# Performance work log

Hardware: AMD Instinct MI355X
Metric: run time of the kernel (lower is better)

The kernel has to match this reference:

```python
import jax, jax.numpy as jnp
import numpy as np

N = 16384   # nodes
E = 262144  # edges (avg degree 16)
H = 256     # hidden_dim
R = 32      # num_radial


def _lin(k, fi, fo):
    return jax.random.normal(k, (fi, fo), jnp.float32) / np.float32(np.sqrt(fi))


def setup_inputs() -> dict:
    key = jax.random.key(0)
    ks = jax.random.split(key, 16)
    h = jax.random.normal(ks[0], (N, H), jnp.float32)
    pos = jax.random.normal(ks[1], (N, 3), jnp.float32)
    edge_index = jax.random.randint(ks[2], (2, E), 0, N, dtype=jnp.int32)
    return {
        'h': h, 'pos': pos,
        # radial_basis: Linear(1,R), SiLU, Linear(R,R)
        'rb_w1': _lin(ks[3], 1, R), 'rb_b1': jnp.zeros((R,), jnp.float32),
        'rb_w2': _lin(ks[4], R, R), 'rb_b2': jnp.zeros((R,), jnp.float32),
        # edge_network: Linear(2H+R,H), SiLU, Linear(H,H), LayerNorm(H)
        'en_w1': _lin(ks[5], 2 * H + R, H), 'en_b1': jnp.zeros((H,), jnp.float32),
        'en_w2': _lin(ks[6], H, H), 'en_b2': jnp.zeros((H,), jnp.float32),
        'en_g': jnp.ones((H,), jnp.float32), 'en_bt': jnp.zeros((H,), jnp.float32),
        # node_network: Linear(2H,H), SiLU, Linear(H,H), LayerNorm(H)
        'nn_w1': _lin(ks[7], 2 * H, H), 'nn_b1': jnp.zeros((H,), jnp.float32),
        'nn_w2': _lin(ks[8], H, H), 'nn_b2': jnp.zeros((H,), jnp.float32),
        'nn_g': jnp.ones((H,), jnp.float32), 'nn_bt': jnp.zeros((H,), jnp.float32),
        # coord_network: Linear(H,H//2), SiLU, Linear(H//2,1), Tanh
        'cn_w1': _lin(ks[9], H, H // 2), 'cn_b1': jnp.zeros((H // 2,), jnp.float32),
        'cn_w2': _lin(ks[10], H // 2, 1), 'cn_b2': jnp.zeros((1,), jnp.float32),
        'edge_index': edge_index,
    }


def _ln(x, g, b, eps=1e-5):
    mu = jnp.mean(x, axis=-1, keepdims=True)
    var = jnp.var(x, axis=-1, keepdims=True)
    return (x - mu) / jnp.sqrt(var + eps) * g + b


def reference(h, pos, rb_w1, rb_b1, rb_w2, rb_b2,
              en_w1, en_b1, en_w2, en_b2, en_g, en_bt,
              nn_w1, nn_b1, nn_w2, nn_b2, nn_g, nn_bt,
              cn_w1, cn_b1, cn_w2, cn_b2, edge_index):
    row, col = edge_index[0], edge_index[1]
    rel_pos = pos[col] - pos[row]                                   # [E,3]
    # torch: norm(rel_pos + 1e-8) -> scalar eps added to the vector first
    dist = jnp.linalg.norm(rel_pos + 1e-8, axis=-1, keepdims=True)  # [E,1]
    radial = jax.nn.silu(dist @ rb_w1 + rb_b1) @ rb_w2 + rb_b2      # [E,R]
    edge_feat = jnp.concatenate([h[row], h[col], radial], axis=-1)  # [E,2H+R]
    edge_msg = _ln(jax.nn.silu(edge_feat @ en_w1 + en_b1) @ en_w2 + en_b2,
                   en_g, en_bt)                                     # [E,H]
    # PyG propagate with aggr='add': sum messages at target nodes (col)
    node_msg = jax.ops.segment_sum(edge_msg, col, num_segments=h.shape[0])
    hn_in = jnp.concatenate([h, node_msg], axis=-1)                 # [N,2H]
    h_updated = _ln(jax.nn.silu(hn_in @ nn_w1 + nn_b1) @ nn_w2 + nn_b2,
                    nn_g, nn_bt)                                    # [N,H]
    coord_w = jnp.tanh(jax.nn.silu(edge_msg @ cn_w1 + cn_b1) @ cn_w2 + cn_b2)  # [E,1]
    weighted = rel_pos * coord_w                                    # [E,3]
    pos_updates = jnp.zeros_like(pos).at[row].add(-weighted).at[col].add(weighted)
    return h_updated, pos_updates
```

## Files before the change

### kernel.cpp

```cpp
#include <hip/hip_runtime.h>
#include <hip/hip_bf16.h>


#define NN 16384
#define EE 262144
#define HH 256
#define RR 32

typedef __bf16 bf16x8 __attribute__((ext_vector_type(8)));
typedef float f32x4 __attribute__((ext_vector_type(4)));

__device__ __forceinline__ float silu_f(float x) { return x / (1.0f + __expf(-x)); }

__device__ __forceinline__ unsigned short bf_bits(float x) {
  union { __hip_bfloat16 b; unsigned short u; } v;
  v.b = __float2bfloat16(x);
  return v.u;
}
__device__ __forceinline__ float ubf(unsigned short u) {
  return __uint_as_float(((unsigned)u) << 16);
}

__global__ __launch_bounds__(256) void conv_h_kernel(const float* __restrict__ src,
                                                     __hip_bfloat16* __restrict__ dst,
                                                     int n4) {
  int i = blockIdx.x * 256 + threadIdx.x;
  if (i >= n4) return;
  float4 v = ((const float4*)src)[i];
  __hip_bfloat16* d = dst + (size_t)i * 4;
  d[0] = __float2bfloat16(v.x);
  d[1] = __float2bfloat16(v.y);
  d[2] = __float2bfloat16(v.z);
  d[3] = __float2bfloat16(v.w);
}

__global__ __launch_bounds__(256) void tr_kernel(const float* __restrict__ in,
                                                 __hip_bfloat16* __restrict__ out,
                                                 int K, int Nc) {
  int i = blockIdx.x * 256 + threadIdx.x;
  if (i >= K * Nc) return;
  int k = i / Nc, c = i - k * Nc;
  out[(size_t)c * K + k] = __float2bfloat16(in[i]);
}

__global__ __launch_bounds__(256) void rwt_kernel(const float* __restrict__ rb_w2,
                                                  const float* __restrict__ en_w1,
                                                  __hip_bfloat16* __restrict__ RWT) {
  int t = blockIdx.x * 256 + threadIdx.x;
  if (t >= 256 * 32) return;
  int c = t >> 5, i = t & 31;
  float s = 0.f;
#pragma unroll
  for (int j = 0; j < 32; ++j) s += rb_w2[i * 32 + j] * en_w1[(512 + j) * 256 + c];
  RWT[c * 32 + i] = __float2bfloat16(s);
}

__global__ __launch_bounds__(256) void b1p_kernel(const float* __restrict__ en_b1,
                                                  const float* __restrict__ rb_b2,
                                                  const float* __restrict__ en_w1,
                                                  float* __restrict__ b1p) {
  int c = blockIdx.x * 256 + threadIdx.x;
  if (c >= 256) return;
  float s = en_b1[c];
#pragma unroll
  for (int j = 0; j < 32; ++j) s += rb_b2[j] * en_w1[(512 + j) * 256 + c];
  b1p[c] = s;
}

__global__ __launch_bounds__(256) void count_kernel(const int* __restrict__ ei,
                                                    int* __restrict__ counts) {
  int e = blockIdx.x * 256 + threadIdx.x;
  if (e >= EE) return;
  atomicAdd(&counts[ei[EE + e]], 1);
}

__global__ __launch_bounds__(256) void scanA_kernel(const int* __restrict__ counts,
                                                    int* __restrict__ bsum) {
  __shared__ int ws[4];
  int t = threadIdx.x;
  int v = counts[blockIdx.x * 256 + t];
#pragma unroll
  for (int m = 1; m < 64; m <<= 1) v += __shfl_xor(v, m, 64);
  if ((t & 63) == 0) ws[t >> 6] = v;
  __syncthreads();
  if (t == 0) bsum[blockIdx.x] = ws[0] + ws[1] + ws[2] + ws[3];
}

__global__ __launch_bounds__(64) void scanB_kernel(const int* __restrict__ bsum,
                                                   int* __restrict__ bbase,
                                                   int* __restrict__ offs) {
  int t = threadIdx.x;
  int v = bsum[t], x = v;
#pragma unroll
  for (int d = 1; d < 64; d <<= 1) {
    int y = __shfl_up(x, d, 64);
    if (t >= d) x += y;
  }
  bbase[t] = x - v;
  if (t == 63) offs[NN] = x;
}

__global__ __launch_bounds__(256) void scanC_kernel(const int* __restrict__ counts,
                                                    const int* __restrict__ bbase,
                                                    int* __restrict__ offs,
                                                    int* __restrict__ cursor) {
  __shared__ int wtot[4];
  int t = threadIdx.x, wv = t >> 6, ln = t & 63;
  int base = blockIdx.x * 256;
  int v = counts[base + t], x = v;
#pragma unroll
  for (int d = 1; d < 64; d <<= 1) {
    int y = __shfl_up(x, d, 64);
    if (ln >= d) x += y;
  }
  if (ln == 63) wtot[wv] = x;
  __syncthreads();
  int add = bbase[blockIdx.x];
  for (int k = 0; k < wv; ++k) add += wtot[k];
  int excl = add + x - v;
  offs[base + t] = excl;
  cursor[base + t] = excl;
}

__global__ __launch_bounds__(256) void scatter_kernel(const int* __restrict__ ei,
                                                      int* __restrict__ cursor,
                                                      int* __restrict__ elist) {
  int e = blockIdx.x * 256 + threadIdx.x;
  if (e >= EE) return;
  int c = ei[EE + e];
  int p = atomicAdd(&cursor[c], 1);
  elist[p] = e;
}

__global__ __launch_bounds__(512) void pgemm_kernel(const __hip_bfloat16* __restrict__ A,
                                                    const __hip_bfloat16* __restrict__ BT,
                                                    __hip_bfloat16* __restrict__ out) {
  const int tid = threadIdx.x, w = tid >> 6, l = tid & 63, r = l & 15, g = l >> 4;
  const int n0 = blockIdx.x * 64;
  f32x4 acc[4][4];
#pragma unroll
  for (int a = 0; a < 4; ++a)
#pragma unroll
    for (int b = 0; b < 4; ++b) acc[a][b] = (f32x4){0.f, 0.f, 0.f, 0.f};
  for (int ks = 0; ks < 8; ++ks) {
    bf16x8 af[4], bfr[4];
#pragma unroll
    for (int fm = 0; fm < 4; ++fm)
      af[fm] = *(const bf16x8*)(A + (size_t)(n0 + fm * 16 + r) * 256 + ks * 32 + g * 8);
#pragma unroll
    for (int fn = 0; fn < 4; ++fn)
      bfr[fn] = *(const bf16x8*)(BT + (size_t)(w * 64 + fn * 16 + r) * 256 + ks * 32 + g * 8);
#pragma unroll
    for (int fm = 0; fm < 4; ++fm)
#pragma unroll
      for (int fn = 0; fn < 4; ++fn)
        acc[fm][fn] =
            __builtin_amdgcn_mfma_f32_16x16x32_bf16(af[fm], bfr[fn], acc[fm][fn], 0, 0, 0);
  }
#pragma unroll
  for (int fm = 0; fm < 4; ++fm)
#pragma unroll
    for (int fn = 0; fn < 4; ++fn) {
      int col = w * 64 + fn * 16 + r;
#pragma unroll
      for (int q = 0; q < 4; ++q) {
        int row = n0 + fm * 16 + g * 4 + q;
        out[(size_t)row * 512 + col] = __float2bfloat16(acc[fm][fn][q]);
      }
    }
}

__global__ __launch_bounds__(512, 4) void edge_kernel(
    const __hip_bfloat16* __restrict__ Pb, const int* __restrict__ ei,
    const float* __restrict__ pos, const float* __restrict__ rb_w1,
    const float* __restrict__ rb_b1, const __hip_bfloat16* __restrict__ RWT,
    const float* __restrict__ b1p, const __hip_bfloat16* __restrict__ W2T,
    const float* __restrict__ en_b2, const float* __restrict__ en_g,
    const float* __restrict__ en_bt, const __hip_bfloat16* __restrict__ CW1T,
    const float* __restrict__ cn_b1, const float* __restrict__ cn_w2,
    const float* __restrict__ cn_b2, const int* __restrict__ elist,
    __hip_bfloat16* __restrict__ emsg, float* __restrict__ pos_out) {
  __shared__ __align__(16) __hip_bfloat16 A2[64 * 264];
  __shared__ float relb[64][3];
  __shared__ float distb[64];
  __shared__ int srow[64], scol[64];
  __shared__ float red[8][64], redsq[8][64];
  __shared__ float mv[64][2];
  __shared__ float cb1b[128], cw2b[128];

  const int tid = threadIdx.x, w = tid >> 6, l = tid & 63, r = l & 15, g = l >> 4;
  const int e0 = blockIdx.x * 64;

  if (tid < 128) {
    cb1b[tid] = cn_b1[tid];
    cw2b[tid] = cn_w2[tid];
  }
  if (tid < 64) {
    int e = elist[e0 + tid];
    int r2 = ei[e], c2 = ei[EE + e];
    srow[tid] = r2;
    scol[tid] = c2;
    float dx = pos[c2 * 3 + 0] - pos[r2 * 3 + 0];
    float dy = pos[c2 * 3 + 1] - pos[r2 * 3 + 1];
    float dz = pos[c2 * 3 + 2] - pos[r2 * 3 + 2];
    relb[tid][0] = dx;
    relb[tid][1] = dy;
    relb[tid][2] = dz;
    float ex = dx + 1e-8f, ey = dy + 1e-8f, ez = dz + 1e-8f;
    distb[tid] = sqrtf(ex * ex + ey * ey + ez * ez);
  }
  __syncthreads();

  unsigned short* A2u = (unsigned short*)A2;
  {
    const int eloc = (w & 3) * 16 + r;
    const int chalf = w >> 2;
    float d = distb[eloc];
    bf16x8 sfrag;
#pragma unroll
    for (int j = 0; j < 8; ++j) {
      float x = d * rb_w1[g * 8 + j] + rb_b1[g * 8 + j];
      sfrag[j] = (__bf16)silu_f(x);
    }
#pragma unroll
    for (int t = 0; t < 8; ++t) {
      int cblk = chalf * 8 + t;
      int cbase = cblk * 16 + g * 4;
      bf16x8 afr = *(const bf16x8*)(RWT + (size_t)(cblk * 16 + r) * 32 + g * 8);
      f32x4 rad = __builtin_amdgcn_mfma_f32_16x16x32_bf16(
          afr, sfrag, (f32x4){0.f, 0.f, 0.f, 0.f}, 0, 0, 0);
      ushort4 o;
      o.x = bf_bits(rad[0]);
      o.y = bf_bits(rad[1]);
      o.z = bf_bits(rad[2]);
      o.w = bf_bits(rad[3]);
      *(ushort4*)(A2u + (size_t)eloc * 264 + cbase) = o;
    }
  }
  __syncthreads();

#pragma unroll
  for (int it = 0; it < 4; ++it) {
    int ch = it * 512 + tid;
    int i = ch >> 5, c = ch & 31;
    bf16x8 radv = *(const bf16x8*)(A2 + i * 264 + c * 8);
    bf16x8 p1 = *(const bf16x8*)(Pb + (size_t)srow[i] * 512 + c * 8);
    bf16x8 p2 = *(const bf16x8*)(Pb + (size_t)scol[i] * 512 + 256 + c * 8);
    float4 b1a = *(const float4*)(b1p + c * 8);
    float4 b1b = *(const float4*)(b1p + c * 8 + 4);
    float bv[8] = {b1a.x, b1a.y, b1a.z, b1a.w, b1b.x, b1b.y, b1b.z, b1b.w};
    bf16x8 o;
#pragma unroll
    for (int j = 0; j < 8; ++j)
      o[j] = (__bf16)silu_f((float)radv[j] + (float)p1[j] + (float)p2[j] + bv[j]);
    *(bf16x8*)(A2 + i * 264 + c * 8) = o;
  }
  __syncthreads();

  f32x4 acc[2][4];
#pragma unroll
  for (int a = 0; a < 2; ++a)
#pragma unroll
    for (int b = 0; b < 4; ++b) acc[a][b] = (f32x4){0.f, 0.f, 0.f, 0.f};
  for (int ks = 0; ks < 8; ++ks) {
    bf16x8 af[2], bfr[4];
#pragma unroll
    for (int mf = 0; mf < 2; ++mf)
      af[mf] = *(const bf16x8*)(W2T + (size_t)(w * 32 + mf * 16 + r) * 256 + ks * 32 + g * 8);
#pragma unroll
    for (int nf = 0; nf < 4; ++nf)
      bfr[nf] = *(const bf16x8*)(A2 + (nf * 16 + r) * 264 + ks * 32 + g * 8);
#pragma unroll
    for (int mf = 0; mf < 2; ++mf)
#pragma unroll
      for (int nf = 0; nf < 4; ++nf)
        acc[mf][nf] =
            __builtin_amdgcn_mfma_f32_16x16x32_bf16(af[mf], bfr[nf], acc[mf][nf], 0, 0, 0);
  }
  {
    float4 b2v0 = *(const float4*)(en_b2 + w * 32 + g * 4);
    float4 b2v1 = *(const float4*)(en_b2 + w * 32 + 16 + g * 4);
#pragma unroll
    for (int nf = 0; nf < 4; ++nf) {
      acc[0][nf][0] += b2v0.x;
      acc[0][nf][1] += b2v0.y;
      acc[0][nf][2] += b2v0.z;
      acc[0][nf][3] += b2v0.w;
      acc[1][nf][0] += b2v1.x;
      acc[1][nf][1] += b2v1.y;
      acc[1][nf][2] += b2v1.z;
      acc[1][nf][3] += b2v1.w;
    }
  }

#pragma unroll
  for (int nf = 0; nf < 4; ++nf) {
    float s = 0.f, sq = 0.f;
#pragma unroll
    for (int mf = 0; mf < 2; ++mf)
#pragma unroll
      for (int q = 0; q < 4; ++q) {
        float v = acc[mf][nf][q];
        s += v;
        sq += v * v;
      }
    s += __shfl_xor(s, 16, 64);
    s += __shfl_xor(s, 32, 64);
    sq += __shfl_xor(sq, 16, 64);
    sq += __shfl_xor(sq, 32, 64);
    if (l < 16) {
      red[w][nf * 16 + l] = s;
      redsq[w][nf * 16 + l] = sq;
    }
  }
  __syncthreads();
  if (tid < 64) {
    float s = 0.f, sq = 0.f;
#pragma unroll
    for (int k = 0; k < 8; ++k) {
      s += red[k][tid];
      sq += redsq[k][tid];
    }
    float mean = s * (1.0f / HH);
    float var = sq * (1.0f / HH) - mean * mean;
    mv[tid][0] = mean;
    mv[tid][1] = rsqrtf(var + 1e-5f);
  }
  __syncthreads();

  {
    float4 gv0 = *(const float4*)(en_g + w * 32 + g * 4);
    float4 gv1 = *(const float4*)(en_g + w * 32 + 16 + g * 4);
    float4 bv0 = *(const float4*)(en_bt + w * 32 + g * 4);
    float4 bv1 = *(const float4*)(en_bt + w * 32 + 16 + g * 4);
#pragma unroll
    for (int nf = 0; nf < 4; ++nf) {
      int e = nf * 16 + r;
      float mm = mv[e][0], rs = mv[e][1];
      ushort4 o0, o1;
      o0.x = bf_bits((acc[0][nf][0] - mm) * rs * gv0.x + bv0.x);
      o0.y = bf_bits((acc[0][nf][1] - mm) * rs * gv0.y + bv0.y);
      o0.z = bf_bits((acc[0][nf][2] - mm) * rs * gv0.z + bv0.z);
      o0.w = bf_bits((acc[0][nf][3] - mm) * rs * gv0.w + bv0.w);
      o1.x = bf_bits((acc[1][nf][0] - mm) * rs * gv1.x + bv1.x);
      o1.y = bf_bits((acc[1][nf][1] - mm) * rs * gv1.y + bv1.y);
      o1.z = bf_bits((acc[1][nf][2] - mm) * rs * gv1.z + bv1.z);
      o1.w = bf_bits((acc[1][nf][3] - mm) * rs * gv1.w + bv1.w);
      *(ushort4*)(A2u + (size_t)e * 264 + w * 32 + g * 4) = o0;
      *(ushort4*)(A2u + (size_t)e * 264 + w * 32 + 16 + g * 4) = o1;
    }
  }
  __syncthreads();

#pragma unroll
  for (int it = 0; it < 4; ++it) {
    int ch = it * 512 + tid;
    int i = ch >> 5, c = ch & 31;
    *(float4*)(emsg + (size_t)(e0 + i) * HH + c * 8) = *(const float4*)(A2 + i * 264 + c * 8);
  }

  f32x4 c2a[4];
#pragma unroll
  for (int a = 0; a < 4; ++a) c2a[a] = (f32x4){0.f, 0.f, 0.f, 0.f};
  for (int ks = 0; ks < 8; ++ks) {
    bf16x8 af[4];
#pragma unroll
    for (int fm = 0; fm < 4; ++fm)
      af[fm] = *(const bf16x8*)(A2 + (fm * 16 + r) * 264 + ks * 32 + g * 8);
    bf16x8 bfr = *(const bf16x8*)(CW1T + (size_t)(w * 16 + r) * 256 + ks * 32 + g * 8);
#pragma unroll
    for (int fm = 0; fm < 4; ++fm)
      c2a[fm] = __builtin_amdgcn_mfma_f32_16x16x32_bf16(af[fm], bfr, c2a[fm], 0, 0, 0);
  }
  {
    int ccol = w * 16 + r;
    float cb = cb1b[ccol], cw = cw2b[ccol];
#pragma unroll
    for (int fm = 0; fm < 4; ++fm)
#pragma unroll
      for (int q = 0; q < 4; ++q) {
        float v = silu_f(c2a[fm][q] + cb) * cw;
#pragma unroll
        for (int m = 1; m < 16; m <<= 1) v += __shfl_xor(v, m, 64);
        if (r == 0) red[w][fm * 16 + g * 4 + q] = v;
      }
  }
  __syncthreads();
  if (tid < 64) {
    float s = cn_b2[0];
#pragma unroll
    for (int k = 0; k < 8; ++k) s += red[k][tid];
    float wgt = tanhf(s);
    float ax = relb[tid][0], ay = relb[tid][1], az = relb[tid][2];
    int rr = srow[tid], cc = scol[tid];
    atomicAdd(&pos_out[rr * 3 + 0], -wgt * ax);
    atomicAdd(&pos_out[rr * 3 + 1], -wgt * ay);
    atomicAdd(&pos_out[rr * 3 + 2], -wgt * az);
    atomicAdd(&pos_out[cc * 3 + 0], wgt * ax);
    atomicAdd(&pos_out[cc * 3 + 1], wgt * ay);
    atomicAdd(&pos_out[cc * 3 + 2], wgt * az);
  }
}

__global__ __launch_bounds__(256) void nodemsg_kernel(const int* __restrict__ offs,
                                                      const __hip_bfloat16* __restrict__ emsg,
                                                      __hip_bfloat16* __restrict__ nmsgb) {
  int wid = threadIdx.x >> 6, l = threadIdx.x & 63;
  int n = blockIdx.x * 4 + wid;
  float a0 = 0.f, a1 = 0.f, a2 = 0.f, a3 = 0.f;
  int b = offs[n], e2 = offs[n + 1];
  const unsigned short* E = (const unsigned short*)emsg;
  int p = b;
  for (; p + 1 < e2; p += 2) {
    ushort4 va = *(const ushort4*)(E + (size_t)p * HH + l * 4);
    ushort4 vb = *(const ushort4*)(E + (size_t)(p + 1) * HH + l * 4);
    a0 += ubf(va.x) + ubf(vb.x);
    a1 += ubf(va.y) + ubf(vb.y);
    a2 += ubf(va.z) + ubf(vb.z);
    a3 += ubf(va.w) + ubf(vb.w);
  }
  if (p < e2) {
    ushort4 va = *(const ushort4*)(E + (size_t)p * HH + l * 4);
    a0 += ubf(va.x);
    a1 += ubf(va.y);
    a2 += ubf(va.z);
    a3 += ubf(va.w);
  }
  ushort4 o;
  o.x = bf_bits(a0);
  o.y = bf_bits(a1);
  o.z = bf_bits(a2);
  o.w = bf_bits(a3);
  *(ushort4*)((unsigned short*)nmsgb + (size_t)n * HH + l * 4) = o;
}

__global__ __launch_bounds__(512, 4) void node_kernel(
    const __hip_bfloat16* __restrict__ hb, const __hip_bfloat16* __restrict__ nmsgb,
    const __hip_bfloat16* __restrict__ NW1T, const float* __restrict__ nn_b1,
    const __hip_bfloat16* __restrict__ NW2T, const float* __restrict__ nn_b2,
    const float* __restrict__ nn_g, const float* __restrict__ nn_bt,
    float* __restrict__ out_h) {
  __shared__ __align__(16) __hip_bfloat16 A2[32 * 264];
  __shared__ float red[8][32], redsq[8][32];
  __shared__ float mv[32][2];
  __shared__ float gb[HH], btb[HH];
  const int tid = threadIdx.x, w = tid >> 6, l = tid & 63, r = l & 15, g = l >> 4;
  const int n0 = blockIdx.x * 32;
  if (tid < 256) {
    gb[tid] = nn_g[tid];
    btb[tid] = nn_bt[tid];
  }

  f32x4 acc[2][2];
#pragma unroll
  for (int a = 0; a < 2; ++a)
#pragma unroll
    for (int b = 0; b < 2; ++b) acc[a][b] = (f32x4){0.f, 0.f, 0.f, 0.f};
  for (int ks = 0; ks < 8; ++ks) {
    bf16x8 af[2], bfr[2];
#pragma unroll
    for (int fm = 0; fm < 2; ++fm)
      af[fm] = *(const bf16x8*)(hb + (size_t)(n0 + fm * 16 + r) * 256 + ks * 32 + g * 8);
#pragma unroll
    for (int fn = 0; fn < 2; ++fn)
      bfr[fn] = *(const bf16x8*)(NW1T + (size_t)(w * 32 + fn * 16 + r) * 512 + ks * 32 + g * 8);
#pragma unroll
    for (int fm = 0; fm < 2; ++fm)
#pragma unroll
      for (int fn = 0; fn < 2; ++fn)
        acc[fm][fn] =
            __builtin_amdgcn_mfma_f32_16x16x32_bf16(af[fm], bfr[fn], acc[fm][fn], 0, 0, 0);
  }
  for (int ks = 0; ks < 8; ++ks) {
    bf16x8 af[2], bfr[2];
#pragma unroll
    for (int fm = 0; fm < 2; ++fm)
      af[fm] = *(const bf16x8*)(nmsgb + (size_t)(n0 + fm * 16 + r) * 256 + ks * 32 + g * 8);
#pragma unroll
    for (int fn = 0; fn < 2; ++fn)
      bfr[fn] =
          *(const bf16x8*)(NW1T + (size_t)(w * 32 + fn * 16 + r) * 512 + 256 + ks * 32 + g * 8);
#pragma unroll
    for (int fm = 0; fm < 2; ++fm)
#pragma unroll
      for (int fn = 0; fn < 2; ++fn)
        acc[fm][fn] =
            __builtin_amdgcn_mfma_f32_16x16x32_bf16(af[fm], bfr[fn], acc[fm][fn], 0, 0, 0);
  }
  __syncthreads();
#pragma unroll
  for (int fn = 0; fn < 2; ++fn) {
    int col = w * 32 + fn * 16 + r;
    float b1 = nn_b1[col];
#pragma unroll
    for (int fm = 0; fm < 2; ++fm)
#pragma unroll
      for (int q = 0; q < 4; ++q) {
        int row = fm * 16 + g * 4 + q;
        A2[row * 264 + col] = __float2bfloat16(silu_f(acc[fm][fn][q] + b1));
      }
  }
  __syncthreads();

#pragma unroll
  for (int a = 0; a < 2; ++a)
#pragma unroll
    for (int b = 0; b < 2; ++b) acc[a][b] = (f32x4){0.f, 0.f, 0.f, 0.f};
  for (int ks = 0; ks < 8; ++ks) {
    bf16x8 af[2], bfr[2];
#pragma unroll
    for (int fm = 0; fm < 2; ++fm)
      af[fm] = *(const bf16x8*)(A2 + (fm * 16 + r) * 264 + ks * 32 + g * 8);
#pragma unroll
    for (int fn = 0; fn < 2; ++fn)
      bfr[fn] = *(const bf16x8*)(NW2T + (size_t)(w * 32 + fn * 16 + r) * 256 + ks * 32 + g * 8);
#pragma unroll
    for (int fm = 0; fm < 2; ++fm)
#pragma unroll
      for (int fn = 0; fn < 2; ++fn)
        acc[fm][fn] =
            __builtin_amdgcn_mfma_f32_16x16x32_bf16(af[fm], bfr[fn], acc[fm][fn], 0, 0, 0);
  }
#pragma unroll
  for (int fn = 0; fn < 2; ++fn) {
    float b2 = nn_b2[w * 32 + fn * 16 + r];
#pragma unroll
    for (int fm = 0; fm < 2; ++fm)
#pragma unroll
      for (int q = 0; q < 4; ++q) acc[fm][fn][q] += b2;
  }
#pragma unroll
  for (int fm = 0; fm < 2; ++fm)
#pragma unroll
    for (int q = 0; q < 4; ++q) {
      float s = acc[fm][0][q] + acc[fm][1][q];
      float sq = acc[fm][0][q] * acc[fm][0][q] + acc[fm][1][q] * acc[fm][1][q];
#pragma unroll
      for (int m = 1; m < 16; m <<= 1) {
        s += __shfl_xor(s, m, 64);
        sq += __shfl_xor(sq, m, 64);
      }
      if (r == 0) {
        red[w][fm * 16 + g * 4 + q] = s;
        redsq[w][fm * 16 + g * 4 + q] = sq;
      }
    }
  __syncthreads();
  if (tid < 32) {
    float s = 0.f, sq = 0.f;
#pragma unroll
    for (int k = 0; k < 8; ++k) {
      s += red[k][tid];
      sq += redsq[k][tid];
    }
    float mean = s * (1.0f / HH);
    float var = sq * (1.0f / HH) - mean * mean;
    mv[tid][0] = mean;
    mv[tid][1] = rsqrtf(var + 1e-5f);
  }
  __syncthreads();
#pragma unroll
  for (int fn = 0; fn < 2; ++fn) {
    int col = w * 32 + fn * 16 + r;
    float gg = gb[col], bb = btb[col];
#pragma unroll
    for (int fm = 0; fm < 2; ++fm)
#pragma unroll
      for (int q = 0; q < 4; ++q) {
        int row = fm * 16 + g * 4 + q;
        out_h[(size_t)(n0 + row) * HH + col] =
            (acc[fm][fn][q] - mv[row][0]) * mv[row][1] * gg + bb;
      }
  }
}

extern "C" void kernel_launch(void* const* d_in, const int* in_sizes, int n_in,
                              void* d_out, int out_size, void* d_ws, size_t ws_size,
                              hipStream_t stream) {
  const float* h = (const float*)d_in[0];
  const float* pos = (const float*)d_in[1];
  const float* rb_w1 = (const float*)d_in[2];
  const float* rb_b1 = (const float*)d_in[3];
  const float* rb_w2 = (const float*)d_in[4];
  const float* rb_b2 = (const float*)d_in[5];
  const float* en_w1 = (const float*)d_in[6];
  const float* en_b1 = (const float*)d_in[7];
  const float* en_w2 = (const float*)d_in[8];
  const float* en_b2 = (const float*)d_in[9];
  const float* en_g = (const float*)d_in[10];
  const float* en_bt = (const float*)d_in[11];
  const float* nn_w1 = (const float*)d_in[12];
  const float* nn_b1 = (const float*)d_in[13];
  const float* nn_w2 = (const float*)d_in[14];
  const float* nn_b2 = (const float*)d_in[15];
  const float* nn_g = (const float*)d_in[16];
  const float* nn_bt = (const float*)d_in[17];
  const float* cn_w1 = (const float*)d_in[18];
  const float* cn_b1 = (const float*)d_in[19];
  const float* cn_w2 = (const float*)d_in[20];
  const float* cn_b2 = (const float*)d_in[21];
  const int* ei = (const int*)d_in[22];

  float* out_h = (float*)d_out;
  float* out_pos = out_h + (size_t)NN * HH;

  char* p = (char*)d_ws;
  auto alloc = [&p](size_t bytes) {
    char* q = p;
    p += (bytes + 255) & ~(size_t)255;
    return q;
  };
  __hip_bfloat16* hb = (__hip_bfloat16*)alloc((size_t)NN * HH * 2);
  __hip_bfloat16* Pb = (__hip_bfloat16*)alloc((size_t)NN * 512 * 2);
  __hip_bfloat16* W1abT = (__hip_bfloat16*)alloc((size_t)512 * 256 * 2);
  __hip_bfloat16* W2T = (__hip_bfloat16*)alloc((size_t)256 * 256 * 2);
  __hip_bfloat16* NW1T = (__hip_bfloat16*)alloc((size_t)256 * 512 * 2);
  __hip_bfloat16* NW2T = (__hip_bfloat16*)alloc((size_t)256 * 256 * 2);
  __hip_bfloat16* CW1T = (__hip_bfloat16*)alloc((size_t)128 * 256 * 2);
  __hip_bfloat16* RWT = (__hip_bfloat16*)alloc((size_t)256 * 32 * 2);
  float* b1p = (float*)alloc((size_t)256 * 4);
  __hip_bfloat16* emsg = (__hip_bfloat16*)alloc((size_t)EE * HH * 2);
  __hip_bfloat16* nmsgb = (__hip_bfloat16*)alloc((size_t)NN * HH * 2);
  int* counts = (int*)alloc((size_t)NN * 4);
  int* offs = (int*)alloc((size_t)(NN + 1) * 4);
  int* cursor = (int*)alloc((size_t)NN * 4);
  int* elist = (int*)alloc((size_t)EE * 4);
  int* bsum = (int*)alloc((size_t)64 * 4);
  int* bbase = (int*)alloc((size_t)64 * 4);

  hipMemsetAsync(out_pos, 0, (size_t)NN * 3 * sizeof(float), stream);
  hipMemsetAsync(counts, 0, (size_t)NN * sizeof(int), stream);

  conv_h_kernel<<<(NN * HH / 4 + 255) / 256, 256, 0, stream>>>(h, hb, NN * HH / 4);
  tr_kernel<<<(256 * 256) / 256, 256, 0, stream>>>(en_w2, W2T, 256, 256);
  tr_kernel<<<(512 * 256) / 256, 256, 0, stream>>>(nn_w1, NW1T, 512, 256);
  tr_kernel<<<(256 * 256) / 256, 256, 0, stream>>>(nn_w2, NW2T, 256, 256);
  tr_kernel<<<(256 * 128) / 256, 256, 0, stream>>>(cn_w1, CW1T, 256, 128);
  tr_kernel<<<(256 * 256) / 256, 256, 0, stream>>>(en_w1, W1abT, 256, 256);
  tr_kernel<<<(256 * 256) / 256, 256, 0, stream>>>(en_w1 + 256 * 256, W1abT + 256 * 256, 256,
                                                   256);
  rwt_kernel<<<(256 * 32) / 256, 256, 0, stream>>>(rb_w2, en_w1, RWT);
  b1p_kernel<<<1, 256, 0, stream>>>(en_b1, rb_b2, en_w1, b1p);
  count_kernel<<<EE / 256, 256, 0, stream>>>(ei, counts);
  scanA_kernel<<<NN / 256, 256, 0, stream>>>(counts, bsum);
  scanB_kernel<<<1, 64, 0, stream>>>(bsum, bbase, offs);
  scanC_kernel<<<NN / 256, 256, 0, stream>>>(counts, bbase, offs, cursor);
  scatter_kernel<<<EE / 256, 256, 0, stream>>>(ei, cursor, elist);
  pgemm_kernel<<<NN / 64, 512, 0, stream>>>(hb, W1abT, Pb);
  edge_kernel<<<EE / 64, 512, 0, stream>>>(Pb, ei, pos, rb_w1, rb_b1, RWT, b1p, W2T, en_b2,
                                           en_g, en_bt, CW1T, cn_b1, cn_w2, cn_b2, elist,
                                           emsg, out_pos);
  nodemsg_kernel<<<NN / 4, 256, 0, stream>>>(offs, emsg, nmsgb);
  node_kernel<<<NN / 32, 512, 0, stream>>>(hb, nmsgb, NW1T, nn_b1, NW2T, nn_b2, nn_g, nn_bt,
                                           out_h);
}
```

Measured before the change: 513.0 us.

## Split edge kernel, fuse segment-sum via atomics, merge weight prep kernels

Merges the weight transpose/prep launches into one kernel. Splits the edge kernel into a hidden-activation kernel that writes a swizzled bf16 buffer and a message kernel that loads it into LDS with global_load_lds. The message kernel reduces sorted-by-target rows in LDS and atomically adds fp32 partial sums into a zeroed node-message buffer, replacing the separate nodemsg pass and the per-edge message write. It also swaps the coord GEMM operand roles and uses XOR swizzle instead of padding. The trade-off is a new E×H intermediate round trip and extra atomics and memset.

```diff
diff --git a/kernel.cpp b/kernel.cpp
--- a/kernel.cpp
+++ b/kernel.cpp
@@ -9,6 +9,13 @@
 
 typedef __bf16 bf16x8 __attribute__((ext_vector_type(8)));
 typedef float f32x4 __attribute__((ext_vector_type(4)));
+
+typedef const void __attribute__((address_space(1)))* gas_ptr;
+typedef void __attribute__((address_space(3)))* las_ptr;
+
+__device__ __forceinline__ void gload16(const void* g, void* l) {
+  __builtin_amdgcn_global_load_lds((gas_ptr)g, (las_ptr)l, 16, 0, 0);
+}
 
 __device__ __forceinline__ float silu_f(float x) { return x / (1.0f + __expf(-x)); }
 
@@ -34,37 +41,48 @@
   d[3] = __float2bfloat16(v.w);
 }
 
-__global__ __launch_bounds__(256) void tr_kernel(const float* __restrict__ in,
-                                                 __hip_bfloat16* __restrict__ out,
-                                                 int K, int Nc) {
-  int i = blockIdx.x * 256 + threadIdx.x;
-  if (i >= K * Nc) return;
-  int k = i / Nc, c = i - k * Nc;
-  out[(size_t)c * K + k] = __float2bfloat16(in[i]);
-}
-
-__global__ __launch_bounds__(256) void rwt_kernel(const float* __restrict__ rb_w2,
-                                                  const float* __restrict__ en_w1,
-                                                  __hip_bfloat16* __restrict__ RWT) {
-  int t = blockIdx.x * 256 + threadIdx.x;
-  if (t >= 256 * 32) return;
-  int c = t >> 5, i = t & 31;
-  float s = 0.f;
-#pragma unroll
-  for (int j = 0; j < 32; ++j) s += rb_w2[i * 32 + j] * en_w1[(512 + j) * 256 + c];
-  RWT[c * 32 + i] = __float2bfloat16(s);
-}
-
-__global__ __launch_bounds__(256) void b1p_kernel(const float* __restrict__ en_b1,
-                                                  const float* __restrict__ rb_b2,
-                                                  const float* __restrict__ en_w1,
-                                                  float* __restrict__ b1p) {
-  int c = blockIdx.x * 256 + threadIdx.x;
-  if (c >= 256) return;
-  float s = en_b1[c];
-#pragma unroll
-  for (int j = 0; j < 32; ++j) s += rb_b2[j] * en_w1[(512 + j) * 256 + c];
-  b1p[c] = s;
+__global__ __launch_bounds__(256) void prep_w_kernel(
+    const float* __restrict__ en_w1, const float* __restrict__ en_w2,
+    const float* __restrict__ nn_w1, const float* __restrict__ nn_w2,
+    const float* __restrict__ cn_w1, const float* __restrict__ rb_w2,
+    const float* __restrict__ rb_b2, const float* __restrict__ en_b1,
+    __hip_bfloat16* __restrict__ W2T, __hip_bfloat16* __restrict__ NW1T,
+    __hip_bfloat16* __restrict__ NW2T, __hip_bfloat16* __restrict__ CW1T,
+    __hip_bfloat16* __restrict__ W1abT, __hip_bfloat16* __restrict__ RWT,
+    float* __restrict__ b1p) {
+  int bid = blockIdx.x, tid = threadIdx.x;
+  if (bid < 256) {
+    int i = bid * 256 + tid, k = i >> 8, c = i & 255;
+    W2T[(size_t)c * 256 + k] = __float2bfloat16(en_w2[i]);
+  } else if (bid < 768) {
+    int i = (bid - 256) * 256 + tid, k = i >> 8, c = i & 255;
+    NW1T[(size_t)c * 512 + k] = __float2bfloat16(nn_w1[i]);
+  } else if (bid < 1024) {
+    int i = (bid - 768) * 256 + tid, k = i >> 8, c = i & 255;
+    NW2T[(size_t)c * 256 + k] = __float2bfloat16(nn_w2[i]);
+  } else if (bid < 1152) {
+    int i = (bid - 1024) * 256 + tid, k = i >> 7, c = i & 127;
+    CW1T[(size_t)c * 256 + k] = __float2bfloat16(cn_w1[i]);
+  } else if (bid < 1408) {
+    int i = (bid - 1152) * 256 + tid, k = i >> 8, c = i & 255;
+    W1abT[(size_t)c * 256 + k] = __float2bfloat16(en_w1[i]);
+  } else if (bid < 1664) {
+    int i = (bid - 1408) * 256 + tid, k = i >> 8, c = i & 255;
+    W1abT[(size_t)(256 + c) * 256 + k] = __float2bfloat16(en_w1[256 * 256 + i]);
+  } else if (bid < 1696) {
+    int t = (bid - 1664) * 256 + tid;
+    int c = t >> 5, i = t & 31;
+    float s = 0.f;
+#pragma unroll
+    for (int j = 0; j < 32; ++j) s += rb_w2[i * 32 + j] * en_w1[(512 + j) * 256 + c];
+    RWT[c * 32 + i] = __float2bfloat16(s);
+  } else {
+    int c = tid;
+    float s = en_b1[c];
+#pragma unroll
+    for (int j = 0; j < 32; ++j) s += rb_b2[j] * en_w1[(512 + j) * 256 + c];
+    b1p[c] = s;
+  }
 }
 
 __global__ __launch_bounds__(256) void count_kernel(const int* __restrict__ ei,
@@ -170,90 +188,79 @@
     }
 }
 
-__global__ __launch_bounds__(512, 4) void edge_kernel(
+__global__ __launch_bounds__(256, 4) void hidden_kernel(
     const __hip_bfloat16* __restrict__ Pb, const int* __restrict__ ei,
     const float* __restrict__ pos, const float* __restrict__ rb_w1,
     const float* __restrict__ rb_b1, const __hip_bfloat16* __restrict__ RWT,
-    const float* __restrict__ b1p, const __hip_bfloat16* __restrict__ W2T,
+    const float* __restrict__ b1p, const int* __restrict__ elist,
+    __hip_bfloat16* __restrict__ hiddenb) {
+  const int tid = threadIdx.x, w = tid >> 6, l = tid & 63, r = l & 15, g = l >> 4;
+  const int slot = blockIdx.x * 64 + w * 16 + r;
+  int e = elist[slot];
+  int nr = ei[e], nc = ei[EE + e];
+  float dx = pos[nc * 3 + 0] - pos[nr * 3 + 0] + 1e-8f;
+  float dy = pos[nc * 3 + 1] - pos[nr * 3 + 1] + 1e-8f;
+  float dz = pos[nc * 3 + 2] - pos[nr * 3 + 2] + 1e-8f;
+  float d = sqrtf(dx * dx + dy * dy + dz * dz);
+  bf16x8 sfrag;
+#pragma unroll
+  for (int j = 0; j < 8; ++j) {
+    float x = d * rb_w1[g * 8 + j] + rb_b1[g * 8 + j];
+    sfrag[j] = (__bf16)silu_f(x);
+  }
+  const unsigned short* Pu = (const unsigned short*)Pb;
+  unsigned short* H = (unsigned short*)hiddenb;
+  const size_t rowbase = (size_t)slot * 256;
+  const int swz = (slot & 7) << 3;
+#pragma unroll 4
+  for (int t = 0; t < 16; ++t) {
+    bf16x8 afr = *(const bf16x8*)(RWT + (size_t)(t * 16 + r) * 32 + g * 8);
+    f32x4 rad = __builtin_amdgcn_mfma_f32_16x16x32_bf16(
+        afr, sfrag, (f32x4){0.f, 0.f, 0.f, 0.f}, 0, 0, 0);
+    int cbase = t * 16 + g * 4;
+    ushort4 p1 = *(const ushort4*)(Pu + (size_t)nr * 512 + cbase);
+    ushort4 p2 = *(const ushort4*)(Pu + (size_t)nc * 512 + 256 + cbase);
+    float4 b1v = *(const float4*)(b1p + cbase);
+    ushort4 o;
+    o.x = bf_bits(silu_f(rad[0] + ubf(p1.x) + ubf(p2.x) + b1v.x));
+    o.y = bf_bits(silu_f(rad[1] + ubf(p1.y) + ubf(p2.y) + b1v.y));
+    o.z = bf_bits(silu_f(rad[2] + ubf(p1.z) + ubf(p2.z) + b1v.z));
+    o.w = bf_bits(silu_f(rad[3] + ubf(p1.w) + ubf(p2.w) + b1v.w));
+    *(ushort4*)(H + rowbase + (cbase ^ swz)) = o;
+  }
+}
+
+__global__ __launch_bounds__(512, 4) void msg_kernel(
+    const __hip_bfloat16* __restrict__ hiddenb, const int* __restrict__ ei,
+    const float* __restrict__ pos, const __hip_bfloat16* __restrict__ W2T,
     const float* __restrict__ en_b2, const float* __restrict__ en_g,
     const float* __restrict__ en_bt, const __hip_bfloat16* __restrict__ CW1T,
     const float* __restrict__ cn_b1, const float* __restrict__ cn_w2,
     const float* __restrict__ cn_b2, const int* __restrict__ elist,
-    __hip_bfloat16* __restrict__ emsg, float* __restrict__ pos_out) {
-  __shared__ __align__(16) __hip_bfloat16 A2[64 * 264];
+    float* __restrict__ nmsg, float* __restrict__ pos_out) {
+  __shared__ __align__(16) __hip_bfloat16 A2[64 * 256];
   __shared__ float relb[64][3];
-  __shared__ float distb[64];
   __shared__ int srow[64], scol[64];
   __shared__ float red[8][64], redsq[8][64];
   __shared__ float mv[64][2];
-  __shared__ float cb1b[128], cw2b[128];
 
   const int tid = threadIdx.x, w = tid >> 6, l = tid & 63, r = l & 15, g = l >> 4;
   const int e0 = blockIdx.x * 64;
-
-  if (tid < 128) {
-    cb1b[tid] = cn_b1[tid];
-    cw2b[tid] = cn_w2[tid];
-  }
+  unsigned short* A2u = (unsigned short*)A2;
+
+#pragma unroll
+  for (int pass = 0; pass < 4; ++pass)
+    gload16((const char*)hiddenb + (size_t)e0 * 512 + pass * 8192 + w * 1024 + l * 16,
+            (char*)A2 + pass * 8192 + w * 1024);
+
   if (tid < 64) {
     int e = elist[e0 + tid];
     int r2 = ei[e], c2 = ei[EE + e];
     srow[tid] = r2;
     scol[tid] = c2;
-    float dx = pos[c2 * 3 + 0] - pos[r2 * 3 + 0];
-    float dy = pos[c2 * 3 + 1] - pos[r2 * 3 + 1];
-    float dz = pos[c2 * 3 + 2] - pos[r2 * 3 + 2];
-    relb[tid][0] = dx;
-    relb[tid][1] = dy;
-    relb[tid][2] = dz;
-    float ex = dx + 1e-8f, ey = dy + 1e-8f, ez = dz + 1e-8f;
-    distb[tid] = sqrtf(ex * ex + ey * ey + ez * ez);
-  }
-  __syncthreads();
-
-  unsigned short* A2u = (unsigned short*)A2;
-  {
-    const int eloc = (w & 3) * 16 + r;
-    const int chalf = w >> 2;
-    float d = distb[eloc];
-    bf16x8 sfrag;
-#pragma unroll
-    for (int j = 0; j < 8; ++j) {
-      float x = d * rb_w1[g * 8 + j] + rb_b1[g * 8 + j];
-      sfrag[j] = (__bf16)silu_f(x);
-    }
-#pragma unroll
-    for (int t = 0; t < 8; ++t) {
-      int cblk = chalf * 8 + t;
-      int cbase = cblk * 16 + g * 4;
-      bf16x8 afr = *(const bf16x8*)(RWT + (size_t)(cblk * 16 + r) * 32 + g * 8);
-      f32x4 rad = __builtin_amdgcn_mfma_f32_16x16x32_bf16(
-          afr, sfrag, (f32x4){0.f, 0.f, 0.f, 0.f}, 0, 0, 0);
-      ushort4 o;
-      o.x = bf_bits(rad[0]);
-      o.y = bf_bits(rad[1]);
-      o.z = bf_bits(rad[2]);
-      o.w = bf_bits(rad[3]);
-      *(ushort4*)(A2u + (size_t)eloc * 264 + cbase) = o;
-    }
-  }
-  __syncthreads();
-
-#pragma unroll
-  for (int it = 0; it < 4; ++it) {
-    int ch = it * 512 + tid;
-    int i = ch >> 5, c = ch & 31;
-    bf16x8 radv = *(const bf16x8*)(A2 + i * 264 + c * 8);
-    bf16x8 p1 = *(const bf16x8*)(Pb + (size_t)srow[i] * 512 + c * 8);
-    bf16x8 p2 = *(const bf16x8*)(Pb + (size_t)scol[i] * 512 + 256 + c * 8);
-    float4 b1a = *(const float4*)(b1p + c * 8);
-    float4 b1b = *(const float4*)(b1p + c * 8 + 4);
-    float bv[8] = {b1a.x, b1a.y, b1a.z, b1a.w, b1b.x, b1b.y, b1b.z, b1b.w};
-    bf16x8 o;
-#pragma unroll
-    for (int j = 0; j < 8; ++j)
-      o[j] = (__bf16)silu_f((float)radv[j] + (float)p1[j] + (float)p2[j] + bv[j]);
-    *(bf16x8*)(A2 + i * 264 + c * 8) = o;
+    relb[tid][0] = pos[c2 * 3 + 0] - pos[r2 * 3 + 0];
+    relb[tid][1] = pos[c2 * 3 + 1] - pos[r2 * 3 + 1];
+    relb[tid][2] = pos[c2 * 3 + 2] - pos[r2 * 3 + 2];
   }
   __syncthreads();
 
@@ -268,8 +275,10 @@
     for (int mf = 0; mf < 2; ++mf)
       af[mf] = *(const bf16x8*)(W2T + (size_t)(w * 32 + mf * 16 + r) * 256 + ks * 32 + g * 8);
 #pragma unroll
-    for (int nf = 0; nf < 4; ++nf)
-      bfr[nf] = *(const bf16x8*)(A2 + (nf * 16 + r) * 264 + ks * 32 + g * 8);
+    for (int nf = 0; nf < 4; ++nf) {
+      int row = nf * 16 + r;
+      bfr[nf] = *(const bf16x8*)(A2 + row * 256 + ((ks * 32 + g * 8) ^ ((row & 7) << 3)));
+    }
 #pragma unroll
     for (int mf = 0; mf < 2; ++mf)
 #pragma unroll
@@ -337,6 +346,7 @@
     for (int nf = 0; nf < 4; ++nf) {
       int e = nf * 16 + r;
       float mm = mv[e][0], rs = mv[e][1];
+      int sz = (e & 7) << 3;
       ushort4 o0, o1;
       o0.x = bf_bits((acc[0][nf][0] - mm) * rs * gv0.x + bv0.x);
       o0.y = bf_bits((acc[0][nf][1] - mm) * rs * gv0.y + bv0.y);
@@ -346,44 +356,57 @@
       o1.y = bf_bits((acc[1][nf][1] - mm) * rs * gv1.y + bv1.y);
       o1.z = bf_bits((acc[1][nf][2] - mm) * rs * gv1.z + bv1.z);
       o1.w = bf_bits((acc[1][nf][3] - mm) * rs * gv1.w + bv1.w);
-      *(ushort4*)(A2u + (size_t)e * 264 + w * 32 + g * 4) = o0;
-      *(ushort4*)(A2u + (size_t)e * 264 + w * 32 + 16 + g * 4) = o1;
-    }
-  }
-  __syncthreads();
-
-#pragma unroll
-  for (int it = 0; it < 4; ++it) {
-    int ch = it * 512 + tid;
-    int i = ch >> 5, c = ch & 31;
-    *(float4*)(emsg + (size_t)(e0 + i) * HH + c * 8) = *(const float4*)(A2 + i * 264 + c * 8);
-  }
-
-  f32x4 c2a[4];
-#pragma unroll
-  for (int a = 0; a < 4; ++a) c2a[a] = (f32x4){0.f, 0.f, 0.f, 0.f};
+      *(ushort4*)(A2u + (size_t)e * 256 + ((w * 32 + g * 4) ^ sz)) = o0;
+      *(ushort4*)(A2u + (size_t)e * 256 + ((w * 32 + 16 + g * 4) ^ sz)) = o1;
+    }
+  }
+  __syncthreads();
+
+  f32x4 cacc[4];
+#pragma unroll
+  for (int a = 0; a < 4; ++a) cacc[a] = (f32x4){0.f, 0.f, 0.f, 0.f};
   for (int ks = 0; ks < 8; ++ks) {
-    bf16x8 af[4];
-#pragma unroll
-    for (int fm = 0; fm < 4; ++fm)
-      af[fm] = *(const bf16x8*)(A2 + (fm * 16 + r) * 264 + ks * 32 + g * 8);
-    bf16x8 bfr = *(const bf16x8*)(CW1T + (size_t)(w * 16 + r) * 256 + ks * 32 + g * 8);
-#pragma unroll
-    for (int fm = 0; fm < 4; ++fm)
-      c2a[fm] = __builtin_amdgcn_mfma_f32_16x16x32_bf16(af[fm], bfr, c2a[fm], 0, 0, 0);
+    bf16x8 af = *(const bf16x8*)(CW1T + (size_t)(w * 16 + r) * 256 + ks * 32 + g * 8);
+    bf16x8 bfr[4];
+#pragma unroll
+    for (int nf = 0; nf < 4; ++nf) {
+      int row = nf * 16 + r;
+      bfr[nf] = *(const bf16x8*)(A2 + row * 256 + ((ks * 32 + g * 8) ^ ((row & 7) << 3)));
+    }
+#pragma unroll
+    for (int nf = 0; nf < 4; ++nf)
+      cacc[nf] = __builtin_amdgcn_mfma_f32_16x16x32_bf16(af, bfr[nf], cacc[nf], 0, 0, 0);
   }
   {
-    int ccol = w * 16 + r;
-    float cb = cb1b[ccol], cw = cw2b[ccol];
-#pragma unroll
-    for (int fm = 0; fm < 4; ++fm)
-#pragma unroll
-      for (int q = 0; q < 4; ++q) {
-        float v = silu_f(c2a[fm][q] + cb) * cw;
-#pragma unroll
-        for (int m = 1; m < 16; m <<= 1) v += __shfl_xor(v, m, 64);
-        if (r == 0) red[w][fm * 16 + g * 4 + q] = v;
+    float4 cb1v = *(const float4*)(cn_b1 + w * 16 + g * 4);
+    float4 cw2v = *(const float4*)(cn_w2 + w * 16 + g * 4);
+#pragma unroll
+    for (int nf = 0; nf < 4; ++nf) {
+      float v = silu_f(cacc[nf][0] + cb1v.x) * cw2v.x +
+                silu_f(cacc[nf][1] + cb1v.y) * cw2v.y +
+                silu_f(cacc[nf][2] + cb1v.z) * cw2v.z +
+                silu_f(cacc[nf][3] + cb1v.w) * cw2v.w;
+      v += __shfl_xor(v, 16, 64);
+      v += __shfl_xor(v, 32, 64);
+      if (l < 16) red[w][nf * 16 + l] = v;
+    }
+  }
+
+  {
+    int c = tid & 255, half = tid >> 8;
+    int rbeg = half * 32, rend = rbeg + 32;
+    float run = 0.f;
+    int cur = scol[rbeg];
+    for (int row = rbeg; row < rend; ++row) {
+      int nd = scol[row];
+      if (nd != cur) {
+        atomicAdd(&nmsg[(size_t)cur * 256 + c], run);
+        run = 0.f;
+        cur = nd;
       }
+      run += ubf(A2u[(size_t)row * 256 + (c ^ ((row & 7) << 3))]);
+    }
+    atomicAdd(&nmsg[(size_t)cur * 256 + c], run);
   }
   __syncthreads();
   if (tid < 64) {
@@ -402,40 +425,8 @@
   }
 }
 
-__global__ __launch_bounds__(256) void nodemsg_kernel(const int* __restrict__ offs,
-                                                      const __hip_bfloat16* __restrict__ emsg,
-                                                      __hip_bfloat16* __restrict__ nmsgb) {
-  int wid = threadIdx.x >> 6, l = threadIdx.x & 63;
-  int n = blockIdx.x * 4 + wid;
-  float a0 = 0.f, a1 = 0.f, a2 = 0.f, a3 = 0.f;
-  int b = offs[n], e2 = offs[n + 1];
-  const unsigned short* E = (const unsigned short*)emsg;
-  int p = b;
-  for (; p + 1 < e2; p += 2) {
-    ushort4 va = *(const ushort4*)(E + (size_t)p * HH + l * 4);
-    ushort4 vb = *(const ushort4*)(E + (size_t)(p + 1) * HH + l * 4);
-    a0 += ubf(va.x) + ubf(vb.x);
-    a1 += ubf(va.y) + ubf(vb.y);
-    a2 += ubf(va.z) + ubf(vb.z);
-    a3 += ubf(va.w) + ubf(vb.w);
-  }
-  if (p < e2) {
-    ushort4 va = *(const ushort4*)(E + (size_t)p * HH + l * 4);
-    a0 += ubf(va.x);
-    a1 += ubf(va.y);
-    a2 += ubf(va.z);
-    a3 += ubf(va.w);
-  }
-  ushort4 o;
-  o.x = bf_bits(a0);
-  o.y = bf_bits(a1);
-  o.z = bf_bits(a2);
-  o.w = bf_bits(a3);
-  *(ushort4*)((unsigned short*)nmsgb + (size_t)n * HH + l * 4) = o;
-}
-
 __global__ __launch_bounds__(512, 4) void node_kernel(
-    const __hip_bfloat16* __restrict__ hb, const __hip_bfloat16* __restrict__ nmsgb,
+    const __hip_bfloat16* __restrict__ hb, const float* __restrict__ nmsg,
     const __hip_bfloat16* __restrict__ NW1T, const float* __restrict__ nn_b1,
     const __hip_bfloat16* __restrict__ NW2T, const float* __restrict__ nn_b2,
     const float* __restrict__ nn_g, const float* __restrict__ nn_bt,
@@ -474,8 +465,21 @@
   for (int ks = 0; ks < 8; ++ks) {
     bf16x8 af[2], bfr[2];
 #pragma unroll
-    for (int fm = 0; fm < 2; ++fm)
-      af[fm] = *(const bf16x8*)(nmsgb + (size_t)(n0 + fm * 16 + r) * 256 + ks * 32 + g * 8);
+    for (int fm = 0; fm < 2; ++fm) {
+      const float* src = nmsg + (size_t)(n0 + fm * 16 + r) * 256 + ks * 32 + g * 8;
+      float4 a0 = *(const float4*)src;
+      float4 a1 = *(const float4*)(src + 4);
+      bf16x8 v;
+      v[0] = (__bf16)a0.x;
+      v[1] = (__bf16)a0.y;
+      v[2] = (__bf16)a0.z;
+      v[3] = (__bf16)a0.w;
+      v[4] = (__bf16)a1.x;
+      v[5] = (__bf16)a1.y;
+      v[6] = (__bf16)a1.z;
+      v[7] = (__bf16)a1.w;
+      af[fm] = v;
+    }
 #pragma unroll
     for (int fn = 0; fn < 2; ++fn)
       bfr[fn] =
@@ -619,8 +623,8 @@
   __hip_bfloat16* CW1T = (__hip_bfloat16*)alloc((size_t)128 * 256 * 2);
   __hip_bfloat16* RWT = (__hip_bfloat16*)alloc((size_t)256 * 32 * 2);
   float* b1p = (float*)alloc((size_t)256 * 4);
-  __hip_bfloat16* emsg = (__hip_bfloat16*)alloc((size_t)EE * HH * 2);
-  __hip_bfloat16* nmsgb = (__hip_bfloat16*)alloc((size_t)NN * HH * 2);
+  __hip_bfloat16* hiddenb = (__hip_bfloat16*)alloc((size_t)EE * HH * 2);
+  float* nmsg = (float*)alloc((size_t)NN * HH * 4);
   int* counts = (int*)alloc((size_t)NN * 4);
   int* offs = (int*)alloc((size_t)(NN + 1) * 4);
   int* cursor = (int*)alloc((size_t)NN * 4);
@@ -630,27 +634,21 @@
 
   hipMemsetAsync(out_pos, 0, (size_t)NN * 3 * sizeof(float), stream);
   hipMemsetAsync(counts, 0, (size_t)NN * sizeof(int), stream);
-
+  hipMemsetAsync(nmsg, 0, (size_t)NN * HH * sizeof(float), stream);
+
+  prep_w_kernel<<<1697, 256, 0, stream>>>(en_w1, en_w2, nn_w1, nn_w2, cn_w1, rb_w2, rb_b2,
+                                          en_b1, W2T, NW1T, NW2T, CW1T, W1abT, RWT, b1p);
   conv_h_kernel<<<(NN * HH / 4 + 255) / 256, 256, 0, stream>>>(h, hb, NN * HH / 4);
-  tr_kernel<<<(256 * 256) / 256, 256, 0, stream>>>(en_w2, W2T, 256, 256);
-  tr_kernel<<<(512 * 256) / 256, 256, 0, stream>>>(nn_w1, NW1T, 512, 256);
-  tr_kernel<<<(256 * 256) / 256, 256, 0, stream>>>(nn_w2, NW2T, 256, 256);
-  tr_kernel<<<(256 * 128) / 256, 256, 0, stream>>>(cn_w1, CW1T, 256, 128);
-  tr_kernel<<<(256 * 256) / 256, 256, 0, stream>>>(en_w1, W1abT, 256, 256);
-  tr_kernel<<<(256 * 256) / 256, 256, 0, stream>>>(en_w1 + 256 * 256, W1abT + 256 * 256, 256,
-                                                   256);
-  rwt_kernel<<<(256 * 32) / 256, 256, 0, stream>>>(rb_w2, en_w1, RWT);
-  b1p_kernel<<<1, 256, 0, stream>>>(en_b1, rb_b2, en_w1, b1p);
   count_kernel<<<EE / 256, 256, 0, stream>>>(ei, counts);
   scanA_kernel<<<NN / 256, 256, 0, stream>>>(counts, bsum);
   scanB_kernel<<<1, 64, 0, stream>>>(bsum, bbase, offs);
   scanC_kernel<<<NN / 256, 256, 0, stream>>>(counts, bbase, offs, cursor);
   scatter_kernel<<<EE / 256, 256, 0, stream>>>(ei, cursor, elist);
   pgemm_kernel<<<NN / 64, 512, 0, stream>>>(hb, W1abT, Pb);
-  edge_kernel<<<EE / 64, 512, 0, stream>>>(Pb, ei, pos, rb_w1, rb_b1, RWT, b1p, W2T, en_b2,
-                                           en_g, en_bt, CW1T, cn_b1, cn_w2, cn_b2, elist,
-                                           emsg, out_pos);
-  nodemsg_kernel<<<NN / 4, 256, 0, stream>>>(offs, emsg, nmsgb);
-  node_kernel<<<NN / 32, 512, 0, stream>>>(hb, nmsgb, NW1T, nn_b1, NW2T, nn_b2, nn_g, nn_bt,
+  hidden_kernel<<<EE / 64, 256, 0, stream>>>(Pb, ei, pos, rb_w1, rb_b1, RWT, b1p, elist,
+                                             hiddenb);
+  msg_kernel<<<EE / 64, 512, 0, stream>>>(hiddenb, ei, pos, W2T, en_b2, en_g, en_bt, CW1T,
+                                          cn_b1, cn_w2, cn_b2, elist, nmsg, out_pos);
+  node_kernel<<<NN / 32, 512, 0, stream>>>(hb, nmsg, NW1T, nn_b1, NW2T, nn_b2, nn_g, nn_bt,
                                            out_h);
 }
```

Measured after the change: 540.8 us. 1.05x slower.
